# Kernel tuning notes

Hardware: AMD Instinct MI355X
Metric: run time of the kernel (lower is better)

Reference implementation:

```python
import jax, jax.numpy as jnp
import numpy as np

NEG = 1e9  # mask value added to already-selected positions (original uses -1e9)


def setup_inputs() -> dict:
    key = jax.random.key(0)
    ks = jax.random.split(key, 12)
    B, N, M = 8, 2048, 256
    s = 0.05  # keep gates/softmax in a sane range
    return dict(
        node_embedding=jax.random.normal(ks[0], (B, N, M), dtype=jnp.float32),
        z_g=jax.random.normal(ks[1], (B, M), dtype=jnp.float32) * s,
        decoder_init=jax.random.normal(ks[2], (M,), dtype=jnp.float32) * s,
        hidden0=jax.random.normal(ks[3], (M,), dtype=jnp.float32) * s,
        w_ih=jax.random.normal(ks[4], (4 * M, M), dtype=jnp.float32) * s,
        w_hh=jax.random.normal(ks[5], (4 * M, M), dtype=jnp.float32) * s,
        b_ih=jax.random.normal(ks[6], (4 * M,), dtype=jnp.float32) * s,
        b_hh=jax.random.normal(ks[7], (4 * M,), dtype=jnp.float32) * s,
        Wq=jax.random.normal(ks[8], (M, M), dtype=jnp.float32) * s,
        bq=jax.random.normal(ks[9], (M,), dtype=jnp.float32) * s,
        Wk=jax.random.normal(ks[10], (M, M), dtype=jnp.float32) * s,
        bk=jax.random.normal(ks[11], (M,), dtype=jnp.float32) * s,
    )


def reference(node_embedding, z_g, decoder_init, hidden0,
              w_ih, w_hh, b_ih, b_hh, Wq, bq, Wk, bk):
    # Returns the per-step masked softmax attention distributions [B, N, N]
    # (row t = distribution over boxes at decode step t; argmax of each row
    #  is the predicted order, and selected indices are masked out).
    N = node_embedding.shape[1]
    # LSTM input is the constant decoder_init every step -> precompute its proj.
    x_proj = decoder_init @ w_ih.T + b_ih  # [4M]

    def decode_one(z_g_b, node_emb_b):
        keys = node_emb_b @ Wk.T + bk  # [N, M] (self.key(node_embedding))

        def step(carry, _):
            h, c, used = carry
            # torch LSTMCell: gates ordered (i, f, g, o)
            gates = x_proj + h @ w_hh.T + b_hh  # [4M]
            i_g, f_g, g_g, o_g = jnp.split(gates, 4)
            i_g = jax.nn.sigmoid(i_g)
            f_g = jax.nn.sigmoid(f_g)
            g_g = jnp.tanh(g_g)
            o_g = jax.nn.sigmoid(o_g)
            c = f_g * c + i_g * g_g
            h = o_g * jnp.tanh(c)
            q = h @ Wq.T + bq                    # [M]
            scores = keys @ q                    # [N]
            scores = jnp.where(used, scores - NEG, scores)  # mask selected
            probs = jax.nn.softmax(scores)       # [N]
            idx = jnp.argmax(probs)              # top-1 pointer selection
            used = used.at[idx].set(True)
            return (h, c, used), probs

        init = (hidden0, z_g_b, jnp.zeros((N,), dtype=bool))
        _, probs = jax.lax.scan(step, init, None, length=N)
        return probs  # [N, N]

    return jax.vmap(decode_one)(z_g, node_embedding)  # [B, N, N]
```

## Files before the change

### kernel.cpp

```cpp
#include <hip/hip_runtime.h>
#include <cstdint>
#include <cstddef>

#define NB 8
#define NN 2048
#define MM 256

typedef unsigned long long u64;

__device__ __forceinline__ unsigned mapf(float f) {
  unsigned u = __float_as_uint(f + 0.f);
  return ((int)u >= 0) ? (u ^ 0x80000000u) : ~u;
}
__device__ __forceinline__ u64 shflx_u64(u64 v, int m) {
  unsigned lo = (unsigned)__shfl_xor((int)(unsigned)v, m);
  unsigned hi = (unsigned)__shfl_xor((int)(v >> 32), m);
  return ((u64)hi << 32) | lo;
}
__device__ __forceinline__ u64 agent_load(const u64* p) {
  return __hip_atomic_load(p, __ATOMIC_RELAXED, __HIP_MEMORY_SCOPE_AGENT);
}

__global__ __launch_bounds__(1024) void lstm_kernel(
    const float* __restrict__ z_g, const float* __restrict__ dec,
    const float* __restrict__ h0, const float* __restrict__ w_ih,
    const float* __restrict__ w_hh, const float* __restrict__ b_ih,
    const float* __restrict__ b_hh, float* __restrict__ Hall,
    u64* __restrict__ Pbuf)
{
  const int b = blockIdx.x;
  const int q = blockIdx.y;
  const int tid = threadIdx.x;
  const int w = tid >> 6;
  const int lane = tid & 63;
  const int rr = lane >> 3;
  const int c8 = lane & 7;
  const int lr = 8 * w + rr;
  const int g = lr >> 5;
  const int m = lr & 31;
  const int grow = g * 256 + 32 * q + m;

  __shared__ __align__(16) float hbuf[256];
  __shared__ __align__(16) float act[128];

  float wreg[32];
  {
    const float* wr = w_hh + (size_t)grow * MM + 32 * c8;
    #pragma unroll
    for (int jj = 0; jj < 8; ++jj) {
      float4 v = *(const float4*)(wr + 4 * ((jj + c8) & 7));
      wreg[4 * jj + 0] = v.x; wreg[4 * jj + 1] = v.y;
      wreg[4 * jj + 2] = v.z; wreg[4 * jj + 3] = v.w;
    }
  }

  float xb;
  {
    const float* wr = w_ih + (size_t)grow * MM + 32 * c8;
    float p = 0.f;
    #pragma unroll
    for (int i = 0; i < 8; ++i) {
      float4 wv = *(const float4*)(wr + 4 * i);
      float4 dv = *(const float4*)(dec + 32 * c8 + 4 * i);
      p += wv.x * dv.x + wv.y * dv.y + wv.z * dv.z + wv.w * dv.w;
    }
    p += __shfl_xor(p, 1); p += __shfl_xor(p, 2); p += __shfl_xor(p, 4);
    xb = p + b_ih[grow] + b_hh[grow];
  }

  float c_my = 0.f;
  if (w == 1 && lane < 32) c_my = z_g[b * MM + 32 * q + lane];
  if (tid < 256) hbuf[tid] = h0[tid];

  u64* Pb = Pbuf + (size_t)b * 512;
  float* Hb = Hall + (size_t)b * NN * MM + 32 * q;

  const bool own0 = ((lane >> 5) + 0) == q;
  const bool own1 = ((lane >> 5) + 2) == q;
  const bool own2 = ((lane >> 5) + 4) == q;
  const bool own3 = ((lane >> 5) + 6) == q;

  for (int tt = 0; tt < NN; ++tt) {
    if (tt > 0 && w == 0) {
      const u64* pa = Pb + ((tt & 1) << 8);
      const unsigned tg = (unsigned)tt;
      u64 a0, a1, a2, a3;
      for (;;) {
        a0 = agent_load(pa + lane);
        a1 = agent_load(pa + 64 + lane);
        a2 = agent_load(pa + 128 + lane);
        a3 = agent_load(pa + 192 + lane);
        const bool ok = (own0 | ((unsigned)(a0 >> 32) == tg))
                      & (own1 | ((unsigned)(a1 >> 32) == tg))
                      & (own2 | ((unsigned)(a2 >> 32) == tg))
                      & (own3 | ((unsigned)(a3 >> 32) == tg));
        if (__all((int)ok)) break;
      }
      if (!own0) hbuf[lane]       = __uint_as_float((unsigned)a0);
      if (!own1) hbuf[64 + lane]  = __uint_as_float((unsigned)a1);
      if (!own2) hbuf[128 + lane] = __uint_as_float((unsigned)a2);
      if (!own3) hbuf[192 + lane] = __uint_as_float((unsigned)a3);
    }
    __syncthreads();

    const float4* h4 = (const float4*)hbuf;
    float a0 = 0.f, a1 = 0.f, a2 = 0.f, a3 = 0.f;
    #pragma unroll
    for (int jj = 0; jj < 8; ++jj) {
      float4 hv = h4[8 * c8 + ((jj + c8) & 7)];
      a0 = fmaf(hv.x, wreg[4 * jj + 0], a0);
      a1 = fmaf(hv.y, wreg[4 * jj + 1], a1);
      a2 = fmaf(hv.z, wreg[4 * jj + 2], a2);
      a3 = fmaf(hv.w, wreg[4 * jj + 3], a3);
    }
    float s = (a0 + a1) + (a2 + a3);
    s += __shfl_xor(s, 1); s += __shfl_xor(s, 2); s += __shfl_xor(s, 4);
    const float gsum = s + xb;

    float a;
    if ((w >> 2) == 2) { const float e = __expf(-2.f * gsum); a = 2.f / (1.f + e) - 1.f; }
    else               { a = 1.f / (1.f + __expf(-gsum)); }
    if (c8 == 0) act[lr] = a;
    __syncthreads();

    if (w == 1 && lane < 32) {
      const float i_g = act[lane], f_g = act[32 + lane];
      const float g_g = act[64 + lane], o_g = act[96 + lane];
      c_my = f_g * c_my + i_g * g_g;
      const float e2 = __expf(-2.f * c_my);
      const float hn = o_g * (2.f / (1.f + e2) - 1.f);
      const u64 pk = ((u64)(unsigned)(tt + 1) << 32) | (u64)__float_as_uint(hn);
      __hip_atomic_store(Pb + (((tt + 1) & 1) << 8) + 32 * q + lane, pk,
                         __ATOMIC_RELAXED, __HIP_MEMORY_SCOPE_AGENT);
      hbuf[32 * q + lane] = hn;
      Hb[(size_t)tt * MM + lane] = hn;
    }
  }
}

__global__ __launch_bounds__(256) void gemm128(
    const float* __restrict__ A, const float* __restrict__ B,
    float* __restrict__ C, const float* __restrict__ bias,
    int K, int Ncol, long sA, long sB, long sC)
{
  __shared__ __align__(16) float As[32][132];
  __shared__ __align__(16) float Bs[32][132];
  const int tid = threadIdx.x;
  const int tx = tid & 15;
  const int ty = tid >> 4;
  const int row0 = blockIdx.y * 128;
  const int col0 = blockIdx.x * 128;
  const float* Ab = A + (size_t)blockIdx.z * (size_t)sA;
  const float* Bb = B + (size_t)blockIdx.z * (size_t)sB;
  float* Cb = C + (size_t)blockIdx.z * (size_t)sC;

  float acc[8][8];
  #pragma unroll
  for (int i = 0; i < 8; ++i)
    #pragma unroll
    for (int jj = 0; jj < 8; ++jj) acc[i][jj] = 0.f;

  for (int k0 = 0; k0 < K; k0 += 32) {
    #pragma unroll
    for (int it = 0; it < 4; ++it) {
      const int idx = tid + it * 256;
      const int r = idx >> 3;
      const int c4 = (idx & 7) << 2;
      float4 va = *(const float4*)(Ab + (size_t)(row0 + r) * K + k0 + c4);
      float4 vb = *(const float4*)(Bb + (size_t)(col0 + r) * K + k0 + c4);
      As[c4 + 0][r] = va.x; As[c4 + 1][r] = va.y;
      As[c4 + 2][r] = va.z; As[c4 + 3][r] = va.w;
      Bs[c4 + 0][r] = vb.x; Bs[c4 + 1][r] = vb.y;
      Bs[c4 + 2][r] = vb.z; Bs[c4 + 3][r] = vb.w;
    }
    __syncthreads();
    #pragma unroll
    for (int kk = 0; kk < 32; ++kk) {
      float4 a0 = *(const float4*)&As[kk][ty * 4];
      float4 a1 = *(const float4*)&As[kk][64 + ty * 4];
      float4 b0 = *(const float4*)&Bs[kk][tx * 4];
      float4 b1 = *(const float4*)&Bs[kk][64 + tx * 4];
      const float av[8] = {a0.x, a0.y, a0.z, a0.w, a1.x, a1.y, a1.z, a1.w};
      const float bv[8] = {b0.x, b0.y, b0.z, b0.w, b1.x, b1.y, b1.z, b1.w};
      #pragma unroll
      for (int i = 0; i < 8; ++i)
        #pragma unroll
        for (int jj = 0; jj < 8; ++jj)
          acc[i][jj] = fmaf(av[i], bv[jj], acc[i][jj]);
    }
    __syncthreads();
  }

  #pragma unroll
  for (int i = 0; i < 8; ++i) {
    const int r = row0 + ((i < 4) ? (ty * 4 + i) : (64 + ty * 4 + i - 4));
    float* cp = Cb + (size_t)r * Ncol + col0;
    float4 o0, o1;
    float* o0p = &o0.x; float* o1p = &o1.x;
    #pragma unroll
    for (int jj = 0; jj < 4; ++jj) {
      float v0 = acc[i][jj], v1 = acc[i][jj + 4];
      if (bias) {
        v0 += bias[col0 + tx * 4 + jj];
        v1 += bias[col0 + 64 + tx * 4 + jj];
      }
      o0p[jj] = v0; o1p[jj] = v1;
    }
    *(float4*)(cp + tx * 4) = o0;
    *(float4*)(cp + 64 + tx * 4) = o1;
  }
}

__global__ __launch_bounds__(512) void select_block(
    const float* __restrict__ S, int* __restrict__ sel)
{
  const int b = blockIdx.x;
  const int tid = threadIdx.x;
  const int w = tid >> 6;
  const int lane = tid & 63;
  const float* Sb = S + (size_t)b * NN * NN + 4 * tid;
  int* selb = sel + b * NN;

  __shared__ u64 partial[2][8];

  for (int i = tid; i < NN; i += 512) selb[i] = 0x7fffffff;
  __syncthreads();

  unsigned mybits = 0;
  const unsigned base = 2047u - 4u * (unsigned)tid;

  auto stepf = [&](float4 v, int t) {
    u64 k0 = (mybits & 1u) ? 0 : (((u64)mapf(v.x) << 32) | (base - 0u));
    u64 k1 = (mybits & 2u) ? 0 : (((u64)mapf(v.y) << 32) | (base - 1u));
    u64 k2 = (mybits & 4u) ? 0 : (((u64)mapf(v.z) << 32) | (base - 2u));
    u64 k3 = (mybits & 8u) ? 0 : (((u64)mapf(v.w) << 32) | (base - 3u));
    u64 k = k0 > k1 ? k0 : k1;
    if (k2 > k) k = k2;
    if (k3 > k) k = k3;
    #pragma unroll
    for (int off = 1; off < 64; off <<= 1) {
      u64 o = shflx_u64(k, off);
      if (o > k) k = o;
    }
    if (lane == 0) partial[t & 1][w] = k;
    __syncthreads();
    u64 pk = partial[t & 1][lane & 7];
    #pragma unroll
    for (int off = 1; off < 8; off <<= 1) {
      u64 o = shflx_u64(pk, off);
      if (o > pk) pk = o;
    }
    const int idx = 2047 - (int)(pk & 0x7ff);
    if ((idx >> 2) == tid) mybits |= 1u << (idx & 3);
    if (tid == 0) selb[idx] = t;
  };

  float4 r0 = *(const float4*)(Sb + (size_t)0 * NN);
  float4 r1 = *(const float4*)(Sb + (size_t)1 * NN);
  float4 r2 = *(const float4*)(Sb + (size_t)2 * NN);
  float4 r3 = *(const float4*)(Sb + (size_t)3 * NN);
  for (int t = 0; t < NN; t += 4) {
    const size_t p4 = (size_t)((t + 4 < NN) ? t + 4 : NN - 1) * NN;
    const size_t p5 = (size_t)((t + 5 < NN) ? t + 5 : NN - 1) * NN;
    const size_t p6 = (size_t)((t + 6 < NN) ? t + 6 : NN - 1) * NN;
    const size_t p7 = (size_t)((t + 7 < NN) ? t + 7 : NN - 1) * NN;
    stepf(r0, t);     r0 = *(const float4*)(Sb + p4);
    stepf(r1, t + 1); r1 = *(const float4*)(Sb + p5);
    stepf(r2, t + 2); r2 = *(const float4*)(Sb + p6);
    stepf(r3, t + 3); r3 = *(const float4*)(Sb + p7);
  }
}

__global__ __launch_bounds__(256) void softmax_kernel(
    float* __restrict__ out, const int* __restrict__ sel)
{
  const int t = blockIdx.x;
  const int b = blockIdx.y;
  const int tid = threadIdx.x;
  float* row = out + ((size_t)b * NN + t) * NN;
  const int* selb = sel + b * NN;
  __shared__ float red[8];

  float v[8];
  int sl[8];
  #pragma unroll
  for (int u = 0; u < 2; ++u) {
    float4 f = *(const float4*)(row + u * 1024 + tid * 4);
    int4 s4 = *(const int4*)(selb + u * 1024 + tid * 4);
    v[u * 4 + 0] = f.x; v[u * 4 + 1] = f.y; v[u * 4 + 2] = f.z; v[u * 4 + 3] = f.w;
    sl[u * 4 + 0] = s4.x; sl[u * 4 + 1] = s4.y; sl[u * 4 + 2] = s4.z; sl[u * 4 + 3] = s4.w;
  }

  float mx = -3.0e38f;
  #pragma unroll
  for (int e = 0; e < 8; ++e)
    if (sl[e] >= t) mx = fmaxf(mx, v[e]);
  #pragma unroll
  for (int off = 1; off < 64; off <<= 1) mx = fmaxf(mx, __shfl_xor(mx, off));
  if ((tid & 63) == 0) red[tid >> 6] = mx;
  __syncthreads();
  mx = fmaxf(fmaxf(red[0], red[1]), fmaxf(red[2], red[3]));

  float e8[8];
  float sum = 0.f;
  #pragma unroll
  for (int e = 0; e < 8; ++e) {
    float ex = (sl[e] >= t) ? __expf(v[e] - mx) : 0.f;
    e8[e] = ex;
    sum += ex;
  }
  #pragma unroll
  for (int off = 1; off < 64; off <<= 1) sum += __shfl_xor(sum, off);
  if ((tid & 63) == 0) red[4 + (tid >> 6)] = sum;
  __syncthreads();
  sum = red[4] + red[5] + red[6] + red[7];
  const float inv = 1.f / sum;

  #pragma unroll
  for (int u = 0; u < 2; ++u) {
    float4 o;
    o.x = e8[u * 4 + 0] * inv; o.y = e8[u * 4 + 1] * inv;
    o.z = e8[u * 4 + 2] * inv; o.w = e8[u * 4 + 3] * inv;
    *(float4*)(row + u * 1024 + tid * 4) = o;
  }
}

extern "C" void kernel_launch(void* const* d_in, const int* in_sizes, int n_in,
                              void* d_out, int out_size, void* d_ws, size_t ws_size,
                              hipStream_t stream)
{
  (void)in_sizes; (void)n_in; (void)out_size; (void)ws_size;
  const float* emb  = (const float*)d_in[0];
  const float* z_g  = (const float*)d_in[1];
  const float* dec  = (const float*)d_in[2];
  const float* h0   = (const float*)d_in[3];
  const float* w_ih = (const float*)d_in[4];
  const float* w_hh = (const float*)d_in[5];
  const float* b_ih = (const float*)d_in[6];
  const float* b_hh = (const float*)d_in[7];
  const float* Wq   = (const float*)d_in[8];
  const float* bq   = (const float*)d_in[9];
  const float* Wk   = (const float*)d_in[10];
  const float* bk   = (const float*)d_in[11];
  float* out = (float*)d_out;
  float* ws  = (float*)d_ws;

  float* keys  = ws;
  float* Q     = ws + 4194304;
  u64*   Pbuf  = (u64*)(ws + 8388608);
  int*   sel   = (int*)(ws + 8396800);
  float* Hall  = out;

  hipMemsetAsync(Pbuf, 0, 4096 * sizeof(u64), stream);

  lstm_kernel<<<dim3(NB, 8), 1024, 0, stream>>>(
      z_g, dec, h0, w_ih, w_hh, b_ih, b_hh, Hall, Pbuf);

  gemm128<<<dim3(MM / 128, (NB * NN) / 128, 1), 256, 0, stream>>>(
      Hall, Wq, Q, bq, MM, MM, 0, 0, 0);

  gemm128<<<dim3(MM / 128, (NB * NN) / 128, 1), 256, 0, stream>>>(
      emb, Wk, keys, bk, MM, MM, 0, 0, 0);

  gemm128<<<dim3(NN / 128, NN / 128, NB), 256, 0, stream>>>(
      Q, keys, out, nullptr, MM, NN,
      (long)NN * MM, (long)NN * MM, (long)NN * NN);

  select_block<<<NB, 512, 0, stream>>>(out, sel);

  softmax_kernel<<<dim3(NN, NB), 256, 0, stream>>>(out, sel);
}
```

Baseline: 4.648 ms.

## Fuse LSTM recurrence with projection and score GEMMs in persistent overlapped kernel

Merges the LSTM recurrence kernel and the three GEMM launches into one persistent kernel. 64 blocks run the recurrent LSTM while the remaining blocks pull tiles from an atomic work queue: key projection first, then Q projection and score tiles gated on release/acquire progress flags posted by the LSTM every 64 steps. The goal is to hide the GEMM work behind the long serial LSTM and to cut launch gaps. The GEMM tile drops to 1024 threads with a 4x4 micro-tile each, and the flag spin-waits add a risk of contention or deadlock if blocks are not co-resident.

```diff
diff --git a/kernel.cpp b/kernel.cpp
--- a/kernel.cpp
+++ b/kernel.cpp
@@ -20,194 +20,265 @@
 __device__ __forceinline__ u64 agent_load(const u64* p) {
   return __hip_atomic_load(p, __ATOMIC_RELAXED, __HIP_MEMORY_SCOPE_AGENT);
 }
-
-__global__ __launch_bounds__(1024) void lstm_kernel(
+__device__ __forceinline__ int acq_load(const int* p) {
+  return __hip_atomic_load(p, __ATOMIC_ACQUIRE, __HIP_MEMORY_SCOPE_AGENT);
+}
+
+__global__ __launch_bounds__(1024) void mega_kernel(
     const float* __restrict__ z_g, const float* __restrict__ dec,
     const float* __restrict__ h0, const float* __restrict__ w_ih,
     const float* __restrict__ w_hh, const float* __restrict__ b_ih,
-    const float* __restrict__ b_hh, float* __restrict__ Hall,
-    u64* __restrict__ Pbuf)
+    const float* __restrict__ b_hh, const float* __restrict__ emb,
+    const float* __restrict__ Wk, const float* __restrict__ bk,
+    const float* __restrict__ Wq, const float* __restrict__ bq,
+    float* __restrict__ keys, float* __restrict__ Qbuf,
+    float* __restrict__ out, u64* __restrict__ Pbuf, int* __restrict__ F)
 {
-  const int b = blockIdx.x;
-  const int q = blockIdx.y;
-  const int tid = threadIdx.x;
-  const int w = tid >> 6;
-  const int lane = tid & 63;
-  const int rr = lane >> 3;
-  const int c8 = lane & 7;
-  const int lr = 8 * w + rr;
-  const int g = lr >> 5;
-  const int m = lr & 31;
-  const int grow = g * 256 + 32 * q + m;
-
   __shared__ __align__(16) float hbuf[256];
   __shared__ __align__(16) float act[128];
-
-  float wreg[32];
-  {
-    const float* wr = w_hh + (size_t)grow * MM + 32 * c8;
-    #pragma unroll
-    for (int jj = 0; jj < 8; ++jj) {
-      float4 v = *(const float4*)(wr + 4 * ((jj + c8) & 7));
-      wreg[4 * jj + 0] = v.x; wreg[4 * jj + 1] = v.y;
-      wreg[4 * jj + 2] = v.z; wreg[4 * jj + 3] = v.w;
-    }
-  }
-
-  float xb;
-  {
-    const float* wr = w_ih + (size_t)grow * MM + 32 * c8;
-    float p = 0.f;
-    #pragma unroll
-    for (int i = 0; i < 8; ++i) {
-      float4 wv = *(const float4*)(wr + 4 * i);
-      float4 dv = *(const float4*)(dec + 32 * c8 + 4 * i);
-      p += wv.x * dv.x + wv.y * dv.y + wv.z * dv.z + wv.w * dv.w;
-    }
-    p += __shfl_xor(p, 1); p += __shfl_xor(p, 2); p += __shfl_xor(p, 4);
-    xb = p + b_ih[grow] + b_hh[grow];
-  }
-
-  float c_my = 0.f;
-  if (w == 1 && lane < 32) c_my = z_g[b * MM + 32 * q + lane];
-  if (tid < 256) hbuf[tid] = h0[tid];
-
-  u64* Pb = Pbuf + (size_t)b * 512;
-  float* Hb = Hall + (size_t)b * NN * MM + 32 * q;
-
-  const bool own0 = ((lane >> 5) + 0) == q;
-  const bool own1 = ((lane >> 5) + 2) == q;
-  const bool own2 = ((lane >> 5) + 4) == q;
-  const bool own3 = ((lane >> 5) + 6) == q;
-
-  for (int tt = 0; tt < NN; ++tt) {
-    if (tt > 0 && w == 0) {
-      const u64* pa = Pb + ((tt & 1) << 8);
-      const unsigned tg = (unsigned)tt;
-      u64 a0, a1, a2, a3;
-      for (;;) {
-        a0 = agent_load(pa + lane);
-        a1 = agent_load(pa + 64 + lane);
-        a2 = agent_load(pa + 128 + lane);
-        a3 = agent_load(pa + 192 + lane);
-        const bool ok = (own0 | ((unsigned)(a0 >> 32) == tg))
-                      & (own1 | ((unsigned)(a1 >> 32) == tg))
-                      & (own2 | ((unsigned)(a2 >> 32) == tg))
-                      & (own3 | ((unsigned)(a3 >> 32) == tg));
-        if (__all((int)ok)) break;
-      }
-      if (!own0) hbuf[lane]       = __uint_as_float((unsigned)a0);
-      if (!own1) hbuf[64 + lane]  = __uint_as_float((unsigned)a1);
-      if (!own2) hbuf[128 + lane] = __uint_as_float((unsigned)a2);
-      if (!own3) hbuf[192 + lane] = __uint_as_float((unsigned)a3);
-    }
-    __syncthreads();
-
-    const float4* h4 = (const float4*)hbuf;
-    float a0 = 0.f, a1 = 0.f, a2 = 0.f, a3 = 0.f;
-    #pragma unroll
-    for (int jj = 0; jj < 8; ++jj) {
-      float4 hv = h4[8 * c8 + ((jj + c8) & 7)];
-      a0 = fmaf(hv.x, wreg[4 * jj + 0], a0);
-      a1 = fmaf(hv.y, wreg[4 * jj + 1], a1);
-      a2 = fmaf(hv.z, wreg[4 * jj + 2], a2);
-      a3 = fmaf(hv.w, wreg[4 * jj + 3], a3);
-    }
-    float s = (a0 + a1) + (a2 + a3);
-    s += __shfl_xor(s, 1); s += __shfl_xor(s, 2); s += __shfl_xor(s, 4);
-    const float gsum = s + xb;
-
-    float a;
-    if ((w >> 2) == 2) { const float e = __expf(-2.f * gsum); a = 2.f / (1.f + e) - 1.f; }
-    else               { a = 1.f / (1.f + __expf(-gsum)); }
-    if (c8 == 0) act[lr] = a;
-    __syncthreads();
-
-    if (w == 1 && lane < 32) {
-      const float i_g = act[lane], f_g = act[32 + lane];
-      const float g_g = act[64 + lane], o_g = act[96 + lane];
-      c_my = f_g * c_my + i_g * g_g;
-      const float e2 = __expf(-2.f * c_my);
-      const float hn = o_g * (2.f / (1.f + e2) - 1.f);
-      const u64 pk = ((u64)(unsigned)(tt + 1) << 32) | (u64)__float_as_uint(hn);
-      __hip_atomic_store(Pb + (((tt + 1) & 1) << 8) + 32 * q + lane, pk,
-                         __ATOMIC_RELAXED, __HIP_MEMORY_SCOPE_AGENT);
-      hbuf[32 * q + lane] = hn;
-      Hb[(size_t)tt * MM + lane] = hn;
-    }
-  }
-}
-
-__global__ __launch_bounds__(256) void gemm128(
-    const float* __restrict__ A, const float* __restrict__ B,
-    float* __restrict__ C, const float* __restrict__ bias,
-    int K, int Ncol, long sA, long sB, long sC)
-{
   __shared__ __align__(16) float As[32][132];
   __shared__ __align__(16) float Bs[32][132];
+  __shared__ int s_tile;
+
   const int tid = threadIdx.x;
-  const int tx = tid & 15;
-  const int ty = tid >> 4;
-  const int row0 = blockIdx.y * 128;
-  const int col0 = blockIdx.x * 128;
-  const float* Ab = A + (size_t)blockIdx.z * (size_t)sA;
-  const float* Bb = B + (size_t)blockIdx.z * (size_t)sB;
-  float* Cb = C + (size_t)blockIdx.z * (size_t)sC;
-
-  float acc[8][8];
-  #pragma unroll
-  for (int i = 0; i < 8; ++i)
+  float* Hall = out;
+
+  if (blockIdx.x < 64) {
+    const int b = blockIdx.x & 7;
+    const int q = blockIdx.x >> 3;
+    const int w = tid >> 6;
+    const int lane = tid & 63;
+    const int rr = lane >> 3;
+    const int c8 = lane & 7;
+    const int lr = 8 * w + rr;
+    const int g = lr >> 5;
+    const int m = lr & 31;
+    const int grow = g * 256 + 32 * q + m;
+
+    float wreg[32];
+    {
+      const float* wr = w_hh + (size_t)grow * MM + 32 * c8;
+      #pragma unroll
+      for (int jj = 0; jj < 8; ++jj) {
+        float4 v = *(const float4*)(wr + 4 * ((jj + c8) & 7));
+        wreg[4 * jj + 0] = v.x; wreg[4 * jj + 1] = v.y;
+        wreg[4 * jj + 2] = v.z; wreg[4 * jj + 3] = v.w;
+      }
+    }
+    float xb;
+    {
+      const float* wr = w_ih + (size_t)grow * MM + 32 * c8;
+      float p = 0.f;
+      #pragma unroll
+      for (int i = 0; i < 8; ++i) {
+        float4 wv = *(const float4*)(wr + 4 * i);
+        float4 dv = *(const float4*)(dec + 32 * c8 + 4 * i);
+        p += wv.x * dv.x + wv.y * dv.y + wv.z * dv.z + wv.w * dv.w;
+      }
+      p += __shfl_xor(p, 1); p += __shfl_xor(p, 2); p += __shfl_xor(p, 4);
+      xb = p + b_ih[grow] + b_hh[grow];
+    }
+
+    float c_my = 0.f;
+    if (w == 1 && lane < 32) c_my = z_g[b * MM + 32 * q + lane];
+    if (tid < 256) hbuf[tid] = h0[tid];
+
+    u64* Pb = Pbuf + (size_t)b * 512;
+    float* Hb = Hall + (size_t)b * NN * MM + 32 * q;
+    int* hflag = F + 8 + (b << 3) + q;
+
+    const bool own0 = ((lane >> 5) + 0) == q;
+    const bool own1 = ((lane >> 5) + 2) == q;
+    const bool own2 = ((lane >> 5) + 4) == q;
+    const bool own3 = ((lane >> 5) + 6) == q;
+
+    for (int tt = 0; tt < NN; ++tt) {
+      if (tt > 0 && w == 0) {
+        const u64* pa = Pb + ((tt & 1) << 8);
+        const unsigned tg = (unsigned)tt;
+        u64 a0, a1, a2, a3;
+        for (;;) {
+          a0 = agent_load(pa + lane);
+          a1 = agent_load(pa + 64 + lane);
+          a2 = agent_load(pa + 128 + lane);
+          a3 = agent_load(pa + 192 + lane);
+          const bool ok = (own0 | ((unsigned)(a0 >> 32) == tg))
+                        & (own1 | ((unsigned)(a1 >> 32) == tg))
+                        & (own2 | ((unsigned)(a2 >> 32) == tg))
+                        & (own3 | ((unsigned)(a3 >> 32) == tg));
+          if (__all((int)ok)) break;
+        }
+        if (!own0) hbuf[lane]       = __uint_as_float((unsigned)a0);
+        if (!own1) hbuf[64 + lane]  = __uint_as_float((unsigned)a1);
+        if (!own2) hbuf[128 + lane] = __uint_as_float((unsigned)a2);
+        if (!own3) hbuf[192 + lane] = __uint_as_float((unsigned)a3);
+      }
+      __syncthreads();
+
+      const float4* h4 = (const float4*)hbuf;
+      float a0 = 0.f, a1 = 0.f, a2 = 0.f, a3 = 0.f;
+      #pragma unroll
+      for (int jj = 0; jj < 8; ++jj) {
+        float4 hv = h4[8 * c8 + ((jj + c8) & 7)];
+        a0 = fmaf(hv.x, wreg[4 * jj + 0], a0);
+        a1 = fmaf(hv.y, wreg[4 * jj + 1], a1);
+        a2 = fmaf(hv.z, wreg[4 * jj + 2], a2);
+        a3 = fmaf(hv.w, wreg[4 * jj + 3], a3);
+      }
+      float s = (a0 + a1) + (a2 + a3);
+      s += __shfl_xor(s, 1); s += __shfl_xor(s, 2); s += __shfl_xor(s, 4);
+      const float gsum = s + xb;
+
+      float a;
+      if ((w >> 2) == 2) { const float e = __expf(-2.f * gsum); a = 2.f / (1.f + e) - 1.f; }
+      else               { a = 1.f / (1.f + __expf(-gsum)); }
+      if (c8 == 0) act[lr] = a;
+      __syncthreads();
+
+      if (w == 1 && lane < 32) {
+        const float i_g = act[lane], f_g = act[32 + lane];
+        const float g_g = act[64 + lane], o_g = act[96 + lane];
+        c_my = f_g * c_my + i_g * g_g;
+        const float e2 = __expf(-2.f * c_my);
+        const float hn = o_g * (2.f / (1.f + e2) - 1.f);
+        const u64 pk = ((u64)(unsigned)(tt + 1) << 32) | (u64)__float_as_uint(hn);
+        __hip_atomic_store(Pb + (((tt + 1) & 1) << 8) + 32 * q + lane, pk,
+                           __ATOMIC_RELAXED, __HIP_MEMORY_SCOPE_AGENT);
+        hbuf[32 * q + lane] = hn;
+        Hb[(size_t)tt * MM + lane] = hn;
+        if (lane == 0 && (tt & 63) == 63)
+          __hip_atomic_store(hflag, tt + 1, __ATOMIC_RELEASE,
+                             __HIP_MEMORY_SCOPE_AGENT);
+      }
+    }
+    if (w == 1 && lane == 0)
+      __hip_atomic_store(hflag, NN, __ATOMIC_RELEASE, __HIP_MEMORY_SCOPE_AGENT);
+    return;
+  }
+
+  int* wcnt  = F;
+  int* hdone = F + 8;
+  int* qdone = F + 80;
+  int* kdone = F + 208;
+
+  for (;;) {
+    __syncthreads();
+    if (tid == 0) s_tile = atomicAdd(wcnt, 1);
+    __syncthreads();
+    const int tile = s_tile;
+    if (tile >= 2560) return;
+
+    const float *Ab, *Bb, *bias;
+    float* Cb; int ldc; int* bumpf = nullptr;
+
+    if (tile < 256) {
+      const int rp = tile >> 1, j = tile & 1;
+      Ab = emb + (size_t)rp * 128 * MM;
+      Bb = Wk + (size_t)j * 128 * MM;
+      bias = bk + j * 128;
+      Cb = keys + (size_t)rp * 128 * MM + j * 128;
+      ldc = MM;
+      bumpf = &kdone[rp];
+    } else if (tile < 2304) {
+      const int t2 = tile - 256;
+      const int i = t2 >> 7;
+      const int r = t2 & 127;
+      if (r < 16) {
+        const int b = r >> 1, j = r & 1;
+        if (tid == 0) {
+          const int need = 128 * (i + 1);
+          for (int qq = 0; qq < 8; ++qq)
+            while (acq_load(&hdone[b * 8 + qq]) < need)
+              __builtin_amdgcn_s_sleep(64);
+        }
+        __syncthreads();
+        Ab = Hall + ((size_t)b * NN + i * 128) * MM;
+        Bb = Wq + (size_t)j * 128 * MM;
+        bias = bq + j * 128;
+        Cb = Qbuf + ((size_t)b * NN + i * 128) * MM + j * 128;
+        ldc = MM;
+        bumpf = &qdone[b * 16 + i];
+      } else {
+        const int rrr = r - 16;
+        const int b = 1 + (rrr >> 4), j = rrr & 15;
+        if (tid == 0) {
+          while (acq_load(&qdone[b * 16 + i]) < 2) __builtin_amdgcn_s_sleep(64);
+          while (acq_load(&kdone[b * 16 + j]) < 2) __builtin_amdgcn_s_sleep(64);
+        }
+        __syncthreads();
+        Ab = Qbuf + ((size_t)b * NN + i * 128) * MM;
+        Bb = keys + ((size_t)b * NN + j * 128) * MM;
+        bias = nullptr;
+        Cb = out + (size_t)b * NN * NN + (size_t)(i * 128) * NN + j * 128;
+        ldc = NN;
+      }
+    } else {
+      const int t3 = tile - 2304;
+      const int i = t3 >> 4, j = t3 & 15;
+      const int bp = i >> 1;
+      if (tid == 0) {
+        for (int t = 0; t < 16; ++t)
+          while (acq_load(&qdone[bp * 16 + t]) < 2) __builtin_amdgcn_s_sleep(64);
+        while (acq_load(&qdone[i]) < 2) __builtin_amdgcn_s_sleep(64);
+        while (acq_load(&kdone[j]) < 2) __builtin_amdgcn_s_sleep(64);
+      }
+      __syncthreads();
+      Ab = Qbuf + (size_t)(i * 128) * MM;
+      Bb = keys + (size_t)(j * 128) * MM;
+      bias = nullptr;
+      Cb = out + (size_t)(i * 128) * NN + j * 128;
+      ldc = NN;
+    }
+
+    const int tx = tid & 31;
+    const int ty = (tid >> 5) & 31;
+    float acc[4][4];
     #pragma unroll
-    for (int jj = 0; jj < 8; ++jj) acc[i][jj] = 0.f;
-
-  for (int k0 = 0; k0 < K; k0 += 32) {
+    for (int ii = 0; ii < 4; ++ii)
+      #pragma unroll
+      for (int jj = 0; jj < 4; ++jj) acc[ii][jj] = 0.f;
+
+    const int sr = tid >> 3;
+    const int sc = (tid & 7) << 2;
+    for (int k0 = 0; k0 < MM; k0 += 32) {
+      float4 va = *(const float4*)(Ab + (size_t)sr * MM + k0 + sc);
+      float4 vb = *(const float4*)(Bb + (size_t)sr * MM + k0 + sc);
+      __syncthreads();
+      As[sc + 0][sr] = va.x; As[sc + 1][sr] = va.y;
+      As[sc + 2][sr] = va.z; As[sc + 3][sr] = va.w;
+      Bs[sc + 0][sr] = vb.x; Bs[sc + 1][sr] = vb.y;
+      Bs[sc + 2][sr] = vb.z; Bs[sc + 3][sr] = vb.w;
+      __syncthreads();
+      #pragma unroll
+      for (int kk = 0; kk < 32; ++kk) {
+        float4 a4 = *(const float4*)&As[kk][ty * 4];
+        float4 b4 = *(const float4*)&Bs[kk][tx * 4];
+        const float av[4] = {a4.x, a4.y, a4.z, a4.w};
+        const float bv[4] = {b4.x, b4.y, b4.z, b4.w};
+        #pragma unroll
+        for (int ii = 0; ii < 4; ++ii)
+          #pragma unroll
+          for (int jj = 0; jj < 4; ++jj)
+            acc[ii][jj] = fmaf(av[ii], bv[jj], acc[ii][jj]);
+      }
+    }
     #pragma unroll
-    for (int it = 0; it < 4; ++it) {
-      const int idx = tid + it * 256;
-      const int r = idx >> 3;
-      const int c4 = (idx & 7) << 2;
-      float4 va = *(const float4*)(Ab + (size_t)(row0 + r) * K + k0 + c4);
-      float4 vb = *(const float4*)(Bb + (size_t)(col0 + r) * K + k0 + c4);
-      As[c4 + 0][r] = va.x; As[c4 + 1][r] = va.y;
-      As[c4 + 2][r] = va.z; As[c4 + 3][r] = va.w;
-      Bs[c4 + 0][r] = vb.x; Bs[c4 + 1][r] = vb.y;
-      Bs[c4 + 2][r] = vb.z; Bs[c4 + 3][r] = vb.w;
-    }
+    for (int ii = 0; ii < 4; ++ii) {
+      float4 o;
+      float* op = &o.x;
+      #pragma unroll
+      for (int jj = 0; jj < 4; ++jj) {
+        float v = acc[ii][jj];
+        if (bias) v += bias[tx * 4 + jj];
+        op[jj] = v;
+      }
+      *(float4*)(Cb + (size_t)(ty * 4 + ii) * ldc + tx * 4) = o;
+    }
+
     __syncthreads();
-    #pragma unroll
-    for (int kk = 0; kk < 32; ++kk) {
-      float4 a0 = *(const float4*)&As[kk][ty * 4];
-      float4 a1 = *(const float4*)&As[kk][64 + ty * 4];
-      float4 b0 = *(const float4*)&Bs[kk][tx * 4];
-      float4 b1 = *(const float4*)&Bs[kk][64 + tx * 4];
-      const float av[8] = {a0.x, a0.y, a0.z, a0.w, a1.x, a1.y, a1.z, a1.w};
-      const float bv[8] = {b0.x, b0.y, b0.z, b0.w, b1.x, b1.y, b1.z, b1.w};
-      #pragma unroll
-      for (int i = 0; i < 8; ++i)
-        #pragma unroll
-        for (int jj = 0; jj < 8; ++jj)
-          acc[i][jj] = fmaf(av[i], bv[jj], acc[i][jj]);
-    }
-    __syncthreads();
-  }
-
-  #pragma unroll
-  for (int i = 0; i < 8; ++i) {
-    const int r = row0 + ((i < 4) ? (ty * 4 + i) : (64 + ty * 4 + i - 4));
-    float* cp = Cb + (size_t)r * Ncol + col0;
-    float4 o0, o1;
-    float* o0p = &o0.x; float* o1p = &o1.x;
-    #pragma unroll
-    for (int jj = 0; jj < 4; ++jj) {
-      float v0 = acc[i][jj], v1 = acc[i][jj + 4];
-      if (bias) {
-        v0 += bias[col0 + tx * 4 + jj];
-        v1 += bias[col0 + 64 + tx * 4 + jj];
-      }
-      o0p[jj] = v0; o1p[jj] = v1;
-    }
-    *(float4*)(cp + tx * 4) = o0;
-    *(float4*)(cp + 64 + tx * 4) = o1;
+    if (bumpf && tid == 0)
+      __hip_atomic_fetch_add(bumpf, 1, __ATOMIC_RELEASE,
+                             __HIP_MEMORY_SCOPE_AGENT);
   }
 }
 
@@ -348,23 +419,14 @@
   float* keys  = ws;
   float* Q     = ws + 4194304;
   u64*   Pbuf  = (u64*)(ws + 8388608);
-  int*   sel   = (int*)(ws + 8396800);
-  float* Hall  = out;
-
-  hipMemsetAsync(Pbuf, 0, 4096 * sizeof(u64), stream);
-
-  lstm_kernel<<<dim3(NB, 8), 1024, 0, stream>>>(
-      z_g, dec, h0, w_ih, w_hh, b_ih, b_hh, Hall, Pbuf);
-
-  gemm128<<<dim3(MM / 128, (NB * NN) / 128, 1), 256, 0, stream>>>(
-      Hall, Wq, Q, bq, MM, MM, 0, 0, 0);
-
-  gemm128<<<dim3(MM / 128, (NB * NN) / 128, 1), 256, 0, stream>>>(
-      emb, Wk, keys, bk, MM, MM, 0, 0, 0);
-
-  gemm128<<<dim3(NN / 128, NN / 128, NB), 256, 0, stream>>>(
-      Q, keys, out, nullptr, MM, NN,
-      (long)NN * MM, (long)NN * MM, (long)NN * NN);
+  int*   F     = (int*)(ws + 8396800);
+  int*   sel   = (int*)(ws + 8397312);
+
+  hipMemsetAsync(Pbuf, 0, 34816, stream);
+
+  mega_kernel<<<256, 1024, 0, stream>>>(
+      z_g, dec, h0, w_ih, w_hh, b_ih, b_hh,
+      emb, Wk, bk, Wq, bq, keys, Q, out, Pbuf, F);
 
   select_block<<<NB, 512, 0, stream>>>(out, sel);
 
```

Result: slower. 5.124 ms (+10.3%).
